# Kernel tuning notes

Hardware: AMD Instinct MI355X
Metric: run time of the kernel (lower is better)

The kernel has to match this reference:

```python
import jax, jax.numpy as jnp
import numpy as np

N, E = 100000, 1600000
IN, H, OUT = 64, 64, 32
BN_EPS = 1e-5


def setup_inputs() -> dict:
    key = jax.random.key(0)
    ks = jax.random.split(key, 13)

    def w(k, shape, fan_in):
        return jax.random.uniform(k, shape, jnp.float32, -1.0, 1.0) / np.sqrt(fan_in)

    return {
        "x": jax.random.normal(ks[0], (N, IN), jnp.float32),
        "edge_index": jax.random.randint(ks[1], (2, E), 0, N, jnp.int32),
        "W1": w(ks[2], (IN, H), IN),
        "b1": jnp.zeros((H,), jnp.float32),
        "gamma": jnp.ones((H,), jnp.float32),
        "beta": jnp.zeros((H,), jnp.float32),
        "W2": w(ks[3], (H, H), H),
        "b2": jnp.zeros((H,), jnp.float32),
        "lin2_w": w(ks[4], (H, OUT), H),
        "lin2_b": w(ks[5], (OUT,), H),
        "lin3_w": w(ks[6], (OUT, H), OUT),
        "lin3_b": w(ks[7], (H,), OUT),
    }


def gcn_conv(x, src, dst, W, b):
    # PyG GCNConv: h = D^{-1/2} (A + I) D^{-1/2} (x W) + b
    n = x.shape[0]
    h = x @ W  # [N, H]
    loop = jnp.arange(n, dtype=src.dtype)
    s = jnp.concatenate([src, loop])  # add self-loops
    d = jnp.concatenate([dst, loop])
    deg = jax.ops.segment_sum(jnp.ones_like(s, x.dtype), d, num_segments=n)
    dinv = jnp.where(deg > 0, jax.lax.rsqrt(deg), 0.0)
    norm = dinv[s] * dinv[d]  # [E+N]
    msg = h[s] * norm[:, None]  # gather + scale
    out = jax.ops.segment_sum(msg, d, num_segments=n)  # scatter-add
    return out + b


def reference(x, edge_index, W1, b1, gamma, beta, W2, b2, lin2_w, lin2_b, lin3_w, lin3_b):
    src, dst = edge_index[0], edge_index[1]
    h = gcn_conv(x, src, dst, W1, b1)
    # BatchNorm1d in eval mode with default running stats (mean=0, var=1)
    h = gamma * (h * jax.lax.rsqrt(jnp.float32(1.0 + BN_EPS))) + beta
    h = jax.nn.relu(h)  # dropout is identity in eval
    h = gcn_conv(h, src, dst, W2, b2)
    logits = h @ lin2_w + lin2_b  # [N, OUT]
    p = jax.nn.softmax(logits, axis=-1)
    ent = -jnp.sum(p * jnp.log(p + 1e-9), axis=-1)  # [N]
    wts = 1.0 / (ent + 1e-10)
    wts = (wts - wts.min()) / (wts.max() - wts.min())
    wts = jax.nn.softmax(wts, axis=0)  # [N]
    graph = jnp.sum(logits * wts[:, None], axis=0, keepdims=True)  # [1, OUT]
    return graph @ lin3_w + lin3_b  # [1, H]
```

## Files before the change

### kernel.cpp

```cpp
#include <hip/hip_runtime.h>
#include <hip/hip_bf16.h>
#include <hip/hip_fp8.h>
#include <math.h>


#define F 64
#define OUTF 32
#define PB 128
#define LEDGE 5632
#define WG 512
#define C1S 24
#define BN_INV 0.9999950000374997f
#define ESC_X 32.0f
#define IESC_X 0.03125f
#define ESC_Z 64.0f
#define IESC_Z 0.015625f

typedef short bf16x8 __attribute__((ext_vector_type(8)));
typedef float f32x4 __attribute__((ext_vector_type(4)));
typedef const __attribute__((address_space(1))) void* gas_ptr;
typedef __attribute__((address_space(3))) void* las_ptr;

__device__ __forceinline__ unsigned short f2bf(float f) {
    unsigned u = __float_as_uint(f);
    return (unsigned short)((u + 0x7fffu + ((u >> 16) & 1u)) >> 16);
}
__device__ __forceinline__ float bf2f(unsigned short h) {
    return __uint_as_float((unsigned)h << 16);
}

#if __has_builtin(__builtin_amdgcn_cvt_f32_fp8) && __has_builtin(__builtin_amdgcn_cvt_pk_fp8_f32)
__device__ __forceinline__ float4 fp8x4(unsigned v) {
    return make_float4(__builtin_amdgcn_cvt_f32_fp8((int)v, 0),
                       __builtin_amdgcn_cvt_f32_fp8((int)v, 1),
                       __builtin_amdgcn_cvt_f32_fp8((int)v, 2),
                       __builtin_amdgcn_cvt_f32_fp8((int)v, 3));
}
__device__ __forceinline__ unsigned fp8pk4(float a, float b, float c, float d) {
    int r = __builtin_amdgcn_cvt_pk_fp8_f32(a, b, 0, false);
    r = __builtin_amdgcn_cvt_pk_fp8_f32(c, d, r, true);
    return (unsigned)r;
}
__device__ __forceinline__ unsigned char fp8enc1(float a) {
    return (unsigned char)(__builtin_amdgcn_cvt_pk_fp8_f32(a, a, 0, false) & 0xff);
}
#else
__device__ __forceinline__ float fp8d1(unsigned char b) {
    __hip_fp8_e4m3 v; v.__x = (__hip_fp8_storage_t)b; return (float)v;
}
__device__ __forceinline__ float4 fp8x4(unsigned v) {
    return make_float4(fp8d1(v & 255u), fp8d1((v >> 8) & 255u), fp8d1((v >> 16) & 255u), fp8d1((v >> 24) & 255u));
}
__device__ __forceinline__ unsigned char fp8enc1(float a) {
    return (unsigned char)__hip_fp8_e4m3(a).__x;
}
__device__ __forceinline__ unsigned fp8pk4(float a, float b, float c, float d) {
    return (unsigned)fp8enc1(a) | ((unsigned)fp8enc1(b) << 8) | ((unsigned)fp8enc1(c) << 16) | ((unsigned)fp8enc1(d) << 24);
}
#endif

__global__ __launch_bounds__(256) void k_hist(const int* __restrict__ dst, int* __restrict__ hist,
                                              int E, int NBK,
                                              const float* __restrict__ W1, const float* __restrict__ b1,
                                              const float* __restrict__ gamma, const float* __restrict__ beta,
                                              const float* __restrict__ W2, const float* __restrict__ b2,
                                              const float* __restrict__ l2w, const float* __restrict__ l2b,
                                              unsigned short* __restrict__ w1f, unsigned short* __restrict__ w2f,
                                              float* __restrict__ bias1f, float* __restrict__ b2l2) {
    __shared__ int lh[512];
    int t = threadIdx.x, blk = blockIdx.x;
    if (blk >= PB) {
        int tt = (blk - PB) * 256 + t;
        int k = tt >> 5, cc = tt & 31;
        float o = 0.0f;
        for (int j = 0; j < F; j++) o += W2[k * F + j] * l2w[j * OUTF + cc];
        {
            int t2 = cc >> 4, s = k >> 5, kb = (k >> 3) & 3, jj = k & 7;
            int ln = kb * 16 + (cc & 15);
            w2f[(size_t)((t2 * 2 + s) * 64 + ln) * 8 + jj] = f2bf(o);
        }
        for (int e = tt; e < F * F; e += 2048) {
            int kk = e >> 6, c = e & 63;
            float wv = W1[kk * F + c] * gamma[c] * BN_INV;
            int t1i = c >> 4, s = kk >> 5, kb = (kk >> 3) & 3, jj = kk & 7;
            int ln = kb * 16 + (c & 15);
            w1f[(size_t)((t1i * 2 + s) * 64 + ln) * 8 + jj] = f2bf(wv);
        }
        if (tt < F) bias1f[tt] = fmaf(b1[tt], gamma[tt] * BN_INV, beta[tt]);
        if (tt < OUTF) {
            float b = l2b[tt];
            for (int j = 0; j < F; j++) b += b2[j] * l2w[j * OUTF + tt];
            b2l2[tt] = b;
        }
        return;
    }
    for (int b = t; b < NBK; b += 256) lh[b] = 0;
    __syncthreads();
    int chunk = (E + PB - 1) / PB;
    int beg = blk * chunk, end = min(beg + chunk, E);
    for (int e = beg + t; e < end; e += 256) atomicAdd(&lh[dst[e] >> 8], 1);
    __syncthreads();
    for (int b = t; b < NBK; b += 256) hist[blk * NBK + b] = lh[b];
}

__global__ __launch_bounds__(PB) void k_hscan1(int* __restrict__ hist, int* __restrict__ btot, int NBK) {
    __shared__ int s[PB];
    int b = blockIdx.x, t = threadIdx.x;
    int v = hist[t * NBK + b];
    s[t] = v;
    __syncthreads();
    for (int off = 1; off < PB; off <<= 1) {
        int u = (t >= off) ? s[t - off] : 0;
        __syncthreads();
        s[t] += u;
        __syncthreads();
    }
    hist[t * NBK + b] = s[t] - v;
    if (t == PB - 1) btot[b] = s[t];
}

__global__ void k_hscan2(const int* __restrict__ btot, int* __restrict__ bbase, int NBK) {
    __shared__ int s[512];
    int t = threadIdx.x;
    int v = (t < NBK) ? btot[t] : 0;
    s[t] = v;
    __syncthreads();
    for (int off = 1; off < 512; off <<= 1) {
        int u = (t >= off) ? s[t - off] : 0;
        __syncthreads();
        s[t] += u;
        __syncthreads();
    }
    if (t < NBK) {
        bbase[t] = s[t] - v;
        if (t == NBK - 1) bbase[NBK] = s[t];
    }
}

__global__ __launch_bounds__(256) void k_place(const int* __restrict__ src, const int* __restrict__ dst,
                                               const int* __restrict__ hist, const int* __restrict__ bbase,
                                               unsigned* __restrict__ bucketArr, int E, int NBK) {
    __shared__ int cur[512];
    int t = threadIdx.x, blk = blockIdx.x;
    for (int b = t; b < NBK; b += 256) cur[b] = hist[blk * NBK + b] + bbase[b];
    __syncthreads();
    int chunk = (E + PB - 1) / PB;
    int beg = blk * chunk, end = min(beg + chunk, E);
    for (int e = beg + t; e < end; e += 256) {
        int d = dst[e], sidx = src[e];
        int p = atomicAdd(&cur[d >> 8], 1);
        bucketArr[p] = ((unsigned)sidx << 8) | (unsigned)(d & 255);
    }
}

__global__ __launch_bounds__(256) void k_binsort(const unsigned* __restrict__ bucketArr,
                                                 const int* __restrict__ bbase,
                                                 int* __restrict__ eidx, int4* __restrict__ meta,
                                                 const float4* __restrict__ x4, unsigned* __restrict__ xq, int N) {
    __shared__ unsigned ledge[LEDGE];
    __shared__ int lcnt[256], lofs[256], lcur[256], lscan[256];
    __shared__ float ldinv[256];
    int b = blockIdx.x, t = threadIdx.x;
    int gb = bbase[b];
    int count = min(bbase[b + 1] - gb, LEDGE);
    for (int j = t; j < count; j += 256) ledge[j] = bucketArr[gb + j];
    lcnt[t] = 0;
    __syncthreads();
    for (int j = t; j < count; j += 256) atomicAdd(&lcnt[ledge[j] & 255u], 1);
    __syncthreads();
    int deg = lcnt[t];
    lscan[t] = deg;
    __syncthreads();
    for (int off = 1; off < 256; off <<= 1) {
        int u = (t >= off) ? lscan[t - off] : 0;
        __syncthreads();
        lscan[t] += u;
        __syncthreads();
    }
    lofs[t] = lscan[t] - deg;
    lcur[t] = 0;
    int node = (b << 8) + t;
    float di = rsqrtf((float)deg + 1.0f);
    ldinv[t] = di;
    if (node < N) meta[node] = make_int4(gb + lofs[t], deg, __float_as_int(di), 0);
    __syncthreads();
    for (int j = t; j < count; j += 256) {
        unsigned v = ledge[j];
        int loc = (int)(v & 255u);
        int p = atomicAdd(&lcur[loc], 1);
        eidx[gb + lofs[loc] + p] = (int)(v >> 8);
    }
    for (int idx = t; idx < 256 * 16; idx += 256) {
        int nd = (b << 8) + (idx >> 4);
        if (nd < N) {
            float d2 = ldinv[idx >> 4] * ESC_X;
            float4 v = x4[(size_t)nd * 16 + (idx & 15)];
            xq[(size_t)nd * 16 + (idx & 15)] = fp8pk4(v.x * d2, v.y * d2, v.z * d2, v.w * d2);
        }
    }
}

__global__ __launch_bounds__(128) void k_conv1l(const char* __restrict__ xqc,
                                                const int4* __restrict__ meta,
                                                const int* __restrict__ eidx,
                                                unsigned short* __restrict__ t1, int N, int Em1) {
    __shared__ __align__(16) unsigned char stage[2][C1S][64 * 16];
    int tid = threadIdx.x, wave = tid >> 6, lane = tid & 63;
    int g = lane >> 2, gl = lane & 3, gbase = lane & 60;
    int i = (blockIdx.x * 2 + wave) * 16 + g;
    int ic = min(i, N - 1);
    int4 m = meta[ic];
    int beg = m.x;
    int dcnt = (i < N) ? m.y : 0;
    float dis = __int_as_float(m.z) * IESC_X;
    int s0 = eidx[min(beg + gl, Em1)];
    int s1 = eidx[min(beg + 4 + gl, Em1)];
    int s2 = eidx[min(beg + 8 + gl, Em1)];
    int s3 = eidx[min(beg + 12 + gl, Em1)];
    int s4 = eidx[min(beg + 16 + gl, Em1)];
    int s5 = eidx[min(beg + 20 + gl, Em1)];
    uint4 selfv = *(const uint4*)(xqc + (size_t)ic * 64 + gl * 16);
#pragma unroll
    for (int k = 0; k < C1S; k++) {
        int sreg = (k < 4) ? s0 : (k < 8) ? s1 : (k < 12) ? s2 : (k < 16) ? s3 : (k < 20) ? s4 : s5;
        int sv = __shfl(sreg, gbase + (k & 3), 64);
        sv = (k < dcnt) ? sv : ic;
        const void* gp = xqc + (size_t)sv * 64 + gl * 16;
        __builtin_amdgcn_global_load_lds((gas_ptr)gp, (las_ptr)&stage[wave][k][0], 16, 0, 0);
    }
    asm volatile("s_waitcnt vmcnt(0)" ::: "memory");
    float4 a0 = fp8x4(selfv.x), a1 = fp8x4(selfv.y), a2 = fp8x4(selfv.z), a3 = fp8x4(selfv.w);
#pragma unroll
    for (int k = 0; k < C1S; k++) {
        if (k < dcnt) {
            uint4 v = *(const uint4*)&stage[wave][k][lane * 16];
            float4 vA = fp8x4(v.x), vB = fp8x4(v.y), vC = fp8x4(v.z), vD = fp8x4(v.w);
            a0.x += vA.x; a0.y += vA.y; a0.z += vA.z; a0.w += vA.w;
            a1.x += vB.x; a1.y += vB.y; a1.z += vB.z; a1.w += vB.w;
            a2.x += vC.x; a2.y += vC.y; a2.z += vC.z; a2.w += vC.w;
            a3.x += vD.x; a3.y += vD.y; a3.z += vD.z; a3.w += vD.w;
        }
    }
    for (int base = C1S; base < dcnt; base += 4) {
        int j = base + gl;
        int ss = eidx[min(beg + j, Em1)];
        int cnt = min(dcnt - base, 4);
#pragma unroll
        for (int k = 0; k < 4; k++) {
            if (k < cnt) {
                int sv = __shfl(ss, gbase + k, 64);
                uint4 v = *(const uint4*)(xqc + (size_t)sv * 64 + gl * 16);
                float4 vA = fp8x4(v.x), vB = fp8x4(v.y), vC = fp8x4(v.z), vD = fp8x4(v.w);
                a0.x += vA.x; a0.y += vA.y; a0.z += vA.z; a0.w += vA.w;
                a1.x += vB.x; a1.y += vB.y; a1.z += vB.z; a1.w += vB.w;
                a2.x += vC.x; a2.y += vC.y; a2.z += vC.z; a2.w += vC.w;
                a3.x += vD.x; a3.y += vD.y; a3.z += vD.z; a3.w += vD.w;
            }
        }
    }
    if (i < N) {
        uint4 o1, o2;
        o1.x = (unsigned)f2bf(a0.x * dis) | ((unsigned)f2bf(a0.y * dis) << 16);
        o1.y = (unsigned)f2bf(a0.z * dis) | ((unsigned)f2bf(a0.w * dis) << 16);
        o1.z = (unsigned)f2bf(a1.x * dis) | ((unsigned)f2bf(a1.y * dis) << 16);
        o1.w = (unsigned)f2bf(a1.z * dis) | ((unsigned)f2bf(a1.w * dis) << 16);
        o2.x = (unsigned)f2bf(a2.x * dis) | ((unsigned)f2bf(a2.y * dis) << 16);
        o2.y = (unsigned)f2bf(a2.z * dis) | ((unsigned)f2bf(a2.w * dis) << 16);
        o2.z = (unsigned)f2bf(a3.x * dis) | ((unsigned)f2bf(a3.y * dis) << 16);
        o2.w = (unsigned)f2bf(a3.z * dis) | ((unsigned)f2bf(a3.w * dis) << 16);
        uint4* outp = (uint4*)(t1 + (size_t)i * F + gl * 16);
        outp[0] = o1;
        outp[1] = o2;
    }
}

__global__ __launch_bounds__(256) void k_zm(const unsigned short* __restrict__ t1bf,
                                            const int4* __restrict__ meta,
                                            const unsigned short* __restrict__ w1f,
                                            const unsigned short* __restrict__ w2f,
                                            const float* __restrict__ bias1f,
                                            unsigned char* __restrict__ z2q, int N) {
    __shared__ __align__(16) unsigned short hlds[4][16][72];
    __shared__ float ldin[4][16];
    int tid = threadIdx.x, wave = tid >> 6, lane = tid & 63;
    int cl = lane & 15, kb = lane >> 4;
    int ntiles = (N + 15) >> 4;
    int tile = blockIdx.x * 4 + wave;
    if (tile >= ntiles) return;
    int row0 = tile << 4;

    int ra = min(row0 + cl, N - 1);
    const bf16x8* arow = (const bf16x8*)(t1bf + (size_t)ra * F);
    bf16x8 a0 = arow[kb];
    bf16x8 a1 = arow[4 + kb];
    if (lane < 16) ldin[wave][lane] = __int_as_float(meta[min(row0 + lane, N - 1)].z);

    const bf16x8* w1v = (const bf16x8*)w1f;
    const bf16x8* w2v = (const bf16x8*)w2f;
    bf16x8 w1frag[8];
#pragma unroll
    for (int q = 0; q < 8; q++) w1frag[q] = w1v[q * 64 + lane];
    bf16x8 w2frag[4];
#pragma unroll
    for (int q = 0; q < 4; q++) w2frag[q] = w2v[q * 64 + lane];
    float bias_t[4];
#pragma unroll
    for (int t = 0; t < 4; t++) bias_t[t] = bias1f[t * 16 + cl];

    f32x4 acc[4] = {};
#pragma unroll
    for (int t = 0; t < 4; t++) {
        acc[t] = __builtin_amdgcn_mfma_f32_16x16x32_bf16(a0, w1frag[t * 2 + 0], acc[t], 0, 0, 0);
        acc[t] = __builtin_amdgcn_mfma_f32_16x16x32_bf16(a1, w1frag[t * 2 + 1], acc[t], 0, 0, 0);
    }
    float di[4];
#pragma unroll
    for (int j = 0; j < 4; j++) di[j] = ldin[wave][kb * 4 + j];
#pragma unroll
    for (int t = 0; t < 4; t++)
#pragma unroll
        for (int j = 0; j < 4; j++) {
            float h = fmaxf(acc[t][j] + bias_t[t], 0.0f) * di[j];
            hlds[wave][kb * 4 + j][t * 16 + cl] = f2bf(h);
        }
    bf16x8 h0 = *(const bf16x8*)&hlds[wave][cl][kb * 8];
    bf16x8 h1 = *(const bf16x8*)&hlds[wave][cl][32 + kb * 8];
    f32x4 accz[2] = {};
#pragma unroll
    for (int t2 = 0; t2 < 2; t2++) {
        accz[t2] = __builtin_amdgcn_mfma_f32_16x16x32_bf16(h0, w2frag[t2 * 2 + 0], accz[t2], 0, 0, 0);
        accz[t2] = __builtin_amdgcn_mfma_f32_16x16x32_bf16(h1, w2frag[t2 * 2 + 1], accz[t2], 0, 0, 0);
    }
#pragma unroll
    for (int t2 = 0; t2 < 2; t2++)
#pragma unroll
        for (int j = 0; j < 4; j++) {
            int r = row0 + kb * 4 + j;
            if (r < N) z2q[(size_t)r * OUTF + t2 * 16 + cl] = fp8enc1(accz[t2][j] * ESC_Z);
        }
}

__device__ __forceinline__ void conv2_consume(const uint2 (&vbuf)[24], uint2 selfv, int dcnt,
                                              int i, int beg, float dis, int gl, int gbase,
                                              const uint2* __restrict__ z2q2, const int* __restrict__ eidx,
                                              int Em1, float4 bvA, float4 bvB,
                                              unsigned short* __restrict__ logits_bf,
                                              float* __restrict__ wraw,
                                              float& mnW, float& mxW, int N) {
    float4 aA0 = fp8x4(selfv.x), aB0 = fp8x4(selfv.y);
    if (i >= N) { aA0 = make_float4(0.f, 0.f, 0.f, 0.f); aB0 = aA0; }
    float4 aA1 = make_float4(0.f, 0.f, 0.f, 0.f), aB1 = aA1;
#pragma unroll
    for (int k = 0; k < 24; k++) {
        if (k < dcnt) {
            float4 vA = fp8x4(vbuf[k].x), vB = fp8x4(vbuf[k].y);
            if (k & 1) {
                aA1.x += vA.x; aA1.y += vA.y; aA1.z += vA.z; aA1.w += vA.w;
                aB1.x += vB.x; aB1.y += vB.y; aB1.z += vB.z; aB1.w += vB.w;
            } else {
                aA0.x += vA.x; aA0.y += vA.y; aA0.z += vA.z; aA0.w += vA.w;
                aB0.x += vB.x; aB0.y += vB.y; aB0.z += vB.z; aB0.w += vB.w;
            }
        }
    }
    for (int base = 24; base < dcnt; base += 4) {
        int j = base + gl;
        int ss = eidx[min(beg + j, Em1)];
        int cnt = min(dcnt - base, 4);
#pragma unroll
        for (int k = 0; k < 4; k++) {
            if (k < cnt) {
                int sv = __shfl(ss, gbase + k, 64);
                uint2 v = z2q2[(size_t)sv * 4 + gl];
                float4 vA = fp8x4(v.x), vB = fp8x4(v.y);
                aA0.x += vA.x; aA0.y += vA.y; aA0.z += vA.z; aA0.w += vA.w;
                aB0.x += vB.x; aB0.y += vB.y; aB0.z += vB.z; aB0.w += vB.w;
            }
        }
    }
    float4 lgA, lgB;
    lgA.x = fmaf(aA0.x + aA1.x, dis, bvA.x);
    lgA.y = fmaf(aA0.y + aA1.y, dis, bvA.y);
    lgA.z = fmaf(aA0.z + aA1.z, dis, bvA.z);
    lgA.w = fmaf(aA0.w + aA1.w, dis, bvA.w);
    lgB.x = fmaf(aB0.x + aB1.x, dis, bvB.x);
    lgB.y = fmaf(aB0.y + aB1.y, dis, bvB.y);
    lgB.z = fmaf(aB0.z + aB1.z, dis, bvB.z);
    lgB.w = fmaf(aB0.w + aB1.w, dis, bvB.w);
    if (i < N) {
        uint4 ob;
        ob.x = (unsigned)f2bf(lgA.x) | ((unsigned)f2bf(lgA.y) << 16);
        ob.y = (unsigned)f2bf(lgA.z) | ((unsigned)f2bf(lgA.w) << 16);
        ob.z = (unsigned)f2bf(lgB.x) | ((unsigned)f2bf(lgB.y) << 16);
        ob.w = (unsigned)f2bf(lgB.z) | ((unsigned)f2bf(lgB.w) << 16);
        *(uint4*)(logits_bf + (size_t)i * OUTF + gl * 8) = ob;
    }
    float m8 = fmaxf(fmaxf(fmaxf(lgA.x, lgA.y), fmaxf(lgA.z, lgA.w)),
                     fmaxf(fmaxf(lgB.x, lgB.y), fmaxf(lgB.z, lgB.w)));
    for (int off = 2; off > 0; off >>= 1) m8 = fmaxf(m8, __shfl_xor(m8, off, 4));
    float p0 = __expf(lgA.x - m8), p1 = __expf(lgA.y - m8), p2 = __expf(lgA.z - m8), p3 = __expf(lgA.w - m8);
    float p4 = __expf(lgB.x - m8), p5 = __expf(lgB.y - m8), p6 = __expf(lgB.z - m8), p7 = __expf(lgB.w - m8);
    float s8 = p0 + p1 + p2 + p3 + p4 + p5 + p6 + p7;
    for (int off = 2; off > 0; off >>= 1) s8 += __shfl_xor(s8, off, 4);
    float inv = 1.0f / s8;
    float t0 = p0 * inv, t1v = p1 * inv, t2v = p2 * inv, t3 = p3 * inv;
    float t4 = p4 * inv, t5 = p5 * inv, t6 = p6 * inv, t7 = p7 * inv;
    float e8 = t0 * __logf(t0 + 1e-9f) + t1v * __logf(t1v + 1e-9f) + t2v * __logf(t2v + 1e-9f) + t3 * __logf(t3 + 1e-9f) +
               t4 * __logf(t4 + 1e-9f) + t5 * __logf(t5 + 1e-9f) + t6 * __logf(t6 + 1e-9f) + t7 * __logf(t7 + 1e-9f);
    for (int off = 2; off > 0; off >>= 1) e8 += __shfl_xor(e8, off, 4);
    float w = 1.0f / (-e8 + 1e-10f);
    if (i < N) {
        if (gl == 0) wraw[i] = w;
        mnW = fminf(mnW, w);
        mxW = fmaxf(mxW, w);
    }
}

__global__ __launch_bounds__(256, 2) void k_conv2agg(const uint2* __restrict__ z2q2,
                                                     const int4* __restrict__ meta,
                                                     const int* __restrict__ eidx, const float* __restrict__ b2l2,
                                                     unsigned short* __restrict__ logits_bf, float* __restrict__ wraw,
                                                     float* __restrict__ mnmx, int N, int Em1) {
    __shared__ float smn[4], smx[4];
    int tid = threadIdx.x, wave = tid >> 6, lane = tid & 63;
    int g = lane >> 2, gl = lane & 3, gbase = lane & 60;
    float4 bvA = ((const float4*)b2l2)[gl * 2];
    float4 bvB = ((const float4*)b2l2)[gl * 2 + 1];
    int wgid = blockIdx.x * 4 + wave;
    int i0 = wgid * 32 + g;
    int i1 = wgid * 32 + 16 + g;
    int i0c = min(i0, N - 1), i1c = min(i1, N - 1);
    int4 m0 = meta[i0c], m1 = meta[i1c];
    int beg0 = m0.x, beg1 = m1.x;
    int d0 = (i0 < N) ? m0.y : 0;
    int d1 = (i1 < N) ? m1.y : 0;
    float dis0 = __int_as_float(m0.z) * IESC_Z;
    float dis1 = __int_as_float(m1.z) * IESC_Z;
    int sA0 = eidx[min(beg0 + gl, Em1)];
    int sA1 = eidx[min(beg0 + 4 + gl, Em1)];
    int sA2 = eidx[min(beg0 + 8 + gl, Em1)];
    int sA3 = eidx[min(beg0 + 12 + gl, Em1)];
    int sA4 = eidx[min(beg0 + 16 + gl, Em1)];
    int sA5 = eidx[min(beg0 + 20 + gl, Em1)];
    int sB0 = eidx[min(beg1 + gl, Em1)];
    int sB1 = eidx[min(beg1 + 4 + gl, Em1)];
    int sB2 = eidx[min(beg1 + 8 + gl, Em1)];
    int sB3 = eidx[min(beg1 + 12 + gl, Em1)];
    int sB4 = eidx[min(beg1 + 16 + gl, Em1)];
    int sB5 = eidx[min(beg1 + 20 + gl, Em1)];
    uint2 self0 = z2q2[(size_t)i0c * 4 + gl];
    uint2 self1 = z2q2[(size_t)i1c * 4 + gl];
    uint2 vb0[24], vb1[24];
#pragma unroll
    for (int k = 0; k < 24; k++) {
        int sreg = (k < 4) ? sA0 : (k < 8) ? sA1 : (k < 12) ? sA2 : (k < 16) ? sA3 : (k < 20) ? sA4 : sA5;
        int sv = __shfl(sreg, gbase + (k & 3), 64);
        sv = (k < d0) ? sv : i0c;
        vb0[k] = z2q2[(size_t)sv * 4 + gl];
    }
#pragma unroll
    for (int k = 0; k < 24; k++) {
        int sreg = (k < 4) ? sB0 : (k < 8) ? sB1 : (k < 12) ? sB2 : (k < 16) ? sB3 : (k < 20) ? sB4 : sB5;
        int sv = __shfl(sreg, gbase + (k & 3), 64);
        sv = (k < d1) ? sv : i1c;
        vb1[k] = z2q2[(size_t)sv * 4 + gl];
    }
    __builtin_amdgcn_sched_barrier(0);
    float mnW = INFINITY, mxW = -INFINITY;
    conv2_consume(vb0, self0, d0, i0, beg0, dis0, gl, gbase, z2q2, eidx, Em1,
                  bvA, bvB, logits_bf, wraw, mnW, mxW, N);
    conv2_consume(vb1, self1, d1, i1, beg1, dis1, gl, gbase, z2q2, eidx, Em1,
                  bvA, bvB, logits_bf, wraw, mnW, mxW, N);
    for (int off = 32; off > 0; off >>= 1) {
        mnW = fminf(mnW, __shfl_xor(mnW, off, 64));
        mxW = fmaxf(mxW, __shfl_xor(mxW, off, 64));
    }
    if (lane == 0) { smn[wave] = mnW; smx[wave] = mxW; }
    __syncthreads();
    if (tid == 0) {
        mnmx[blockIdx.x * 2]     = fminf(fminf(smn[0], smn[1]), fminf(smn[2], smn[3]));
        mnmx[blockIdx.x * 2 + 1] = fmaxf(fmaxf(smx[0], smx[1]), fmaxf(smx[2], smx[3]));
    }
}

__global__ __launch_bounds__(256) void k_weight(const unsigned short* __restrict__ logits_bf,
                                                const float* __restrict__ wraw,
                                                const float* __restrict__ mnmx, int nmm,
                                                float* __restrict__ part, int N) {
    __shared__ float rmn[4], rmx[4];
    float mn = INFINITY, mx = -INFINITY;
    for (int j = threadIdx.x; j < nmm; j += 256) {
        mn = fminf(mn, mnmx[j * 2]);
        mx = fmaxf(mx, mnmx[j * 2 + 1]);
    }
    for (int off = 32; off > 0; off >>= 1) {
        mn = fminf(mn, __shfl_xor(mn, off, 64));
        mx = fmaxf(mx, __shfl_xor(mx, off, 64));
    }
    int wv = threadIdx.x >> 6;
    if ((threadIdx.x & 63) == 0) { rmn[wv] = mn; rmx[wv] = mx; }
    __syncthreads();
    mn = fminf(fminf(rmn[0], rmn[1]), fminf(rmn[2], rmn[3]));
    mx = fmaxf(fmaxf(rmx[0], rmx[1]), fmaxf(rmx[2], rmx[3]));
    float inv = 1.0f / (mx - mn);
    int c = threadIdx.x & 31;
    int g = threadIdx.x >> 5;
    float acc = 0.0f, es = 0.0f;
    for (int r = blockIdx.x * 8 + g; r < N; r += gridDim.x * 8) {
        float e = __expf((wraw[r] - mn) * inv);
        acc += e * bf2f(logits_bf[(size_t)r * OUTF + c]);
        if (c == 0) es += e;
    }
    __shared__ float sa[8][OUTF];
    __shared__ float se[8];
    sa[g][c] = acc;
    if (c == 0) se[g] = es;
    __syncthreads();
    if (g == 0) {
        float t = sa[0][c];
#pragma unroll
        for (int i = 1; i < 8; i++) t += sa[i][c];
        part[blockIdx.x * 36 + c] = t;
        if (c == 0) {
            float u = 0.0f;
#pragma unroll
            for (int i = 0; i < 8; i++) u += se[i];
            part[blockIdx.x * 36 + 32] = u;
        }
    }
}

__global__ __launch_bounds__(256) void k_final(const float* __restrict__ part,
                                               const float* __restrict__ w3, const float* __restrict__ b3,
                                               float* __restrict__ out) {
    __shared__ float sa[8][OUTF];
    __shared__ float se[8];
    __shared__ float facc[OUTF + 1];
    int tid = threadIdx.x;
    int g = tid >> 5, c = tid & 31;
    float acc = 0.0f, es = 0.0f;
    for (int p = g; p < WG; p += 8) {
        acc += part[p * 36 + c];
        if (c == 0) es += part[p * 36 + 32];
    }
    sa[g][c] = acc;
    if (c == 0) se[g] = es;
    __syncthreads();
    if (tid < OUTF) {
        float t = 0.0f;
#pragma unroll
        for (int i = 0; i < 8; i++) t += sa[i][tid];
        facc[tid] = t;
    }
    if (tid == 32) {
        float u = 0.0f;
#pragma unroll
        for (int i = 0; i < 8; i++) u += se[i];
        facc[OUTF] = u;
    }
    __syncthreads();
    if (tid < F) {
        float s = facc[OUTF];
        float o = b3[tid];
#pragma unroll
        for (int cc = 0; cc < OUTF; cc++) o += (facc[cc] / s) * w3[cc * F + tid];
        out[tid] = o;
    }
}

extern "C" void kernel_launch(void* const* d_in, const int* in_sizes, int n_in,
                              void* d_out, int out_size, void* d_ws, size_t ws_size,
                              hipStream_t stream) {
    const float* x     = (const float*)d_in[0];
    const int*   ei    = (const int*)d_in[1];
    const float* W1    = (const float*)d_in[2];
    const float* b1    = (const float*)d_in[3];
    const float* gamma = (const float*)d_in[4];
    const float* beta  = (const float*)d_in[5];
    const float* W2    = (const float*)d_in[6];
    const float* b2    = (const float*)d_in[7];
    const float* l2w   = (const float*)d_in[8];
    const float* l2b   = (const float*)d_in[9];
    const float* l3w   = (const float*)d_in[10];
    const float* l3b   = (const float*)d_in[11];

    int N = in_sizes[0] / F;
    int E = in_sizes[1] / 2;
    const int* src = ei;
    const int* dst = ei + E;
    int NBK = (N + 255) >> 8;

    char* p = (char*)d_ws;
    int* hist = (int*)p;                p += (size_t)PB * NBK * 4;
    int* btot = (int*)p;                p += 512 * 4;
    int* bbase = (int*)p;               p += 516 * 4;
    unsigned* bucketArr = (unsigned*)p; p += (size_t)E * 4;
    int4* meta = (int4*)p;              p += (size_t)N * 16;
    int* eidx = (int*)p;                p += (size_t)E * 4;
    float* mnmx = (float*)p;            p += 2048 * 4;
    float* part = (float*)p;            p += (size_t)WG * 36 * 4;
    unsigned short* w1f = (unsigned short*)p;  p += F * F * 2;
    unsigned short* w2f = (unsigned short*)p;  p += F * OUTF * 2;
    float* bias1f = (float*)p;          p += F * 4;
    float* b2l2 = (float*)p;            p += OUTF * 4 + 32;
    unsigned* xq = (unsigned*)p;        p += (size_t)N * F;
    unsigned short* t1bf = (unsigned short*)p; p += (size_t)N * F * 2;
    float* wraw = (float*)p;            p += (size_t)N * 4;
    unsigned char* z2q = (unsigned char*)xq;
    unsigned short* logits_bf = (unsigned short*)t1bf;

    k_hist<<<PB + 8, 256, 0, stream>>>(dst, hist, E, NBK, W1, b1, gamma, beta, W2, b2, l2w, l2b,
                                       w1f, w2f, bias1f, b2l2);
    k_hscan1<<<NBK, PB, 0, stream>>>(hist, btot, NBK);
    k_hscan2<<<1, 512, 0, stream>>>(btot, bbase, NBK);
    k_place<<<PB, 256, 0, stream>>>(src, dst, hist, bbase, bucketArr, E, NBK);
    k_binsort<<<NBK, 256, 0, stream>>>(bucketArr, bbase, eidx, meta, (const float4*)x, xq, N);

    int nb1 = (N + 31) / 32;
    k_conv1l<<<nb1, 128, 0, stream>>>((const char*)xq, meta, eidx, t1bf, N, E - 1);
    int nt = (N + 15) >> 4;
    k_zm<<<(nt + 3) / 4, 256, 0, stream>>>(t1bf, meta, w1f, w2f, bias1f, z2q, N);
    int wg2 = (nt + 1) >> 1;
    int nb2 = (wg2 + 3) >> 2;
    k_conv2agg<<<nb2, 256, 0, stream>>>((const uint2*)z2q, meta, eidx, b2l2, logits_bf, wraw, mnmx, N, E - 1);

    k_weight<<<WG, 256, 0, stream>>>(logits_bf, wraw, mnmx, nb2, part, N);
    k_final<<<1, 256, 0, stream>>>(part, l3w, l3b, (float*)d_out);
}
```

Measured before the change: 246.6 us.

## Fuse conv1 aggregation with dense transform and inline bucket-total scan

Merges the first-layer gather/aggregation kernel with the MFMA transform kernel so the aggregated row tile stays in shared memory instead of round-tripping through a bf16 global buffer. It also removes the single-block bucket-total scan kernel and recomputes that scan redundantly inside each block of the placement and binsort kernels with a wave-shuffle scan. Gathers for absent neighbours are now skipped instead of loading the self row. The trade-offs are two fewer launches and less global traffic, against more registers and shared memory in the fused kernel and a repeated small scan in every block.

```diff
diff --git a/kernel.cpp b/kernel.cpp
--- a/kernel.cpp
+++ b/kernel.cpp
@@ -58,6 +58,34 @@
     return (unsigned)fp8enc1(a) | ((unsigned)fp8enc1(b) << 8) | ((unsigned)fp8enc1(c) << 16) | ((unsigned)fp8enc1(d) << 24);
 }
 #endif
+
+__device__ __forceinline__ void scan_btot(const int* __restrict__ btot, int* sbase, int NBK, int tid) {
+    if (tid < 64) {
+        int lane = tid;
+        int vals[8];
+        int lsum = 0;
+#pragma unroll
+        for (int q = 0; q < 8; q++) {
+            int idx = lane * 8 + q;
+            int v = (idx < NBK) ? btot[idx] : 0;
+            vals[q] = lsum;
+            lsum += v;
+        }
+        int run = lsum;
+        for (int off = 1; off < 64; off <<= 1) {
+            int u = __shfl_up(run, off, 64);
+            if (lane >= off) run += u;
+        }
+        int excl = run - lsum;
+#pragma unroll
+        for (int q = 0; q < 8; q++) {
+            int idx = lane * 8 + q;
+            if (idx <= NBK) sbase[idx] = excl + vals[q];
+        }
+        if (lane == 63) sbase[NBK] = run;
+    }
+    __syncthreads();
+}
 
 __global__ __launch_bounds__(256) void k_hist(const int* __restrict__ dst, int* __restrict__ hist,
                                               int E, int NBK,
@@ -119,30 +147,14 @@
     if (t == PB - 1) btot[b] = s[t];
 }
 
-__global__ void k_hscan2(const int* __restrict__ btot, int* __restrict__ bbase, int NBK) {
-    __shared__ int s[512];
-    int t = threadIdx.x;
-    int v = (t < NBK) ? btot[t] : 0;
-    s[t] = v;
-    __syncthreads();
-    for (int off = 1; off < 512; off <<= 1) {
-        int u = (t >= off) ? s[t - off] : 0;
-        __syncthreads();
-        s[t] += u;
-        __syncthreads();
-    }
-    if (t < NBK) {
-        bbase[t] = s[t] - v;
-        if (t == NBK - 1) bbase[NBK] = s[t];
-    }
-}
-
 __global__ __launch_bounds__(256) void k_place(const int* __restrict__ src, const int* __restrict__ dst,
-                                               const int* __restrict__ hist, const int* __restrict__ bbase,
+                                               const int* __restrict__ hist, const int* __restrict__ btot,
                                                unsigned* __restrict__ bucketArr, int E, int NBK) {
     __shared__ int cur[512];
+    __shared__ int sbase[513];
     int t = threadIdx.x, blk = blockIdx.x;
-    for (int b = t; b < NBK; b += 256) cur[b] = hist[blk * NBK + b] + bbase[b];
+    scan_btot(btot, sbase, NBK, t);
+    for (int b = t; b < NBK; b += 256) cur[b] = hist[blk * NBK + b] + sbase[b];
     __syncthreads();
     int chunk = (E + PB - 1) / PB;
     int beg = blk * chunk, end = min(beg + chunk, E);
@@ -154,15 +166,17 @@
 }
 
 __global__ __launch_bounds__(256) void k_binsort(const unsigned* __restrict__ bucketArr,
-                                                 const int* __restrict__ bbase,
+                                                 const int* __restrict__ btot,
                                                  int* __restrict__ eidx, int4* __restrict__ meta,
-                                                 const float4* __restrict__ x4, unsigned* __restrict__ xq, int N) {
+                                                 const float4* __restrict__ x4, unsigned* __restrict__ xq, int N, int NBK) {
     __shared__ unsigned ledge[LEDGE];
     __shared__ int lcnt[256], lofs[256], lcur[256], lscan[256];
+    __shared__ int sbase[513];
     __shared__ float ldinv[256];
     int b = blockIdx.x, t = threadIdx.x;
-    int gb = bbase[b];
-    int count = min(bbase[b + 1] - gb, LEDGE);
+    scan_btot(btot, sbase, NBK, t);
+    int gb = sbase[b];
+    int count = min(sbase[b + 1] - gb, LEDGE);
     for (int j = t; j < count; j += 256) ledge[j] = bucketArr[gb + j];
     lcnt[t] = 0;
     __syncthreads();
@@ -200,11 +214,16 @@
     }
 }
 
-__global__ __launch_bounds__(128) void k_conv1l(const char* __restrict__ xqc,
-                                                const int4* __restrict__ meta,
-                                                const int* __restrict__ eidx,
-                                                unsigned short* __restrict__ t1, int N, int Em1) {
+__global__ __launch_bounds__(128) void k_c1z(const char* __restrict__ xqc,
+                                             const int4* __restrict__ meta,
+                                             const int* __restrict__ eidx,
+                                             const unsigned short* __restrict__ w1f,
+                                             const unsigned short* __restrict__ w2f,
+                                             const float* __restrict__ bias1f,
+                                             unsigned char* __restrict__ z2q, int N, int Em1) {
     __shared__ __align__(16) unsigned char stage[2][C1S][64 * 16];
+    __shared__ __align__(16) unsigned short tile[2][16][72];
+    __shared__ float ldin[2][16];
     int tid = threadIdx.x, wave = tid >> 6, lane = tid & 63;
     int g = lane >> 2, gl = lane & 3, gbase = lane & 60;
     int i = (blockIdx.x * 2 + wave) * 16 + g;
@@ -213,6 +232,7 @@
     int beg = m.x;
     int dcnt = (i < N) ? m.y : 0;
     float dis = __int_as_float(m.z) * IESC_X;
+    if (gl == 0) ldin[wave][g] = __int_as_float(m.z);
     int s0 = eidx[min(beg + gl, Em1)];
     int s1 = eidx[min(beg + 4 + gl, Em1)];
     int s2 = eidx[min(beg + 8 + gl, Em1)];
@@ -224,12 +244,25 @@
     for (int k = 0; k < C1S; k++) {
         int sreg = (k < 4) ? s0 : (k < 8) ? s1 : (k < 12) ? s2 : (k < 16) ? s3 : (k < 20) ? s4 : s5;
         int sv = __shfl(sreg, gbase + (k & 3), 64);
-        sv = (k < dcnt) ? sv : ic;
-        const void* gp = xqc + (size_t)sv * 64 + gl * 16;
-        __builtin_amdgcn_global_load_lds((gas_ptr)gp, (las_ptr)&stage[wave][k][0], 16, 0, 0);
-    }
+        if (k < dcnt) {
+            const void* gp = xqc + (size_t)sv * 64 + gl * 16;
+            __builtin_amdgcn_global_load_lds((gas_ptr)gp, (las_ptr)&stage[wave][k][0], 16, 0, 0);
+        }
+    }
+    int cl = lane & 15, kb = lane >> 4;
+    const bf16x8* w1v = (const bf16x8*)w1f;
+    const bf16x8* w2v = (const bf16x8*)w2f;
+    bf16x8 w1frag[8];
+#pragma unroll
+    for (int q = 0; q < 8; q++) w1frag[q] = w1v[q * 64 + lane];
+    bf16x8 w2frag[4];
+#pragma unroll
+    for (int q = 0; q < 4; q++) w2frag[q] = w2v[q * 64 + lane];
+    float bias_t[4];
+#pragma unroll
+    for (int t = 0; t < 4; t++) bias_t[t] = bias1f[t * 16 + cl];
+    float4 a0 = fp8x4(selfv.x), a1 = fp8x4(selfv.y), a2 = fp8x4(selfv.z), a3 = fp8x4(selfv.w);
     asm volatile("s_waitcnt vmcnt(0)" ::: "memory");
-    float4 a0 = fp8x4(selfv.x), a1 = fp8x4(selfv.y), a2 = fp8x4(selfv.z), a3 = fp8x4(selfv.w);
 #pragma unroll
     for (int k = 0; k < C1S; k++) {
         if (k < dcnt) {
@@ -258,7 +291,7 @@
             }
         }
     }
-    if (i < N) {
+    {
         uint4 o1, o2;
         o1.x = (unsigned)f2bf(a0.x * dis) | ((unsigned)f2bf(a0.y * dis) << 16);
         o1.y = (unsigned)f2bf(a0.z * dis) | ((unsigned)f2bf(a0.w * dis) << 16);
@@ -268,50 +301,17 @@
         o2.y = (unsigned)f2bf(a2.z * dis) | ((unsigned)f2bf(a2.w * dis) << 16);
         o2.z = (unsigned)f2bf(a3.x * dis) | ((unsigned)f2bf(a3.y * dis) << 16);
         o2.w = (unsigned)f2bf(a3.z * dis) | ((unsigned)f2bf(a3.w * dis) << 16);
-        uint4* outp = (uint4*)(t1 + (size_t)i * F + gl * 16);
-        outp[0] = o1;
-        outp[1] = o2;
-    }
-}
-
-__global__ __launch_bounds__(256) void k_zm(const unsigned short* __restrict__ t1bf,
-                                            const int4* __restrict__ meta,
-                                            const unsigned short* __restrict__ w1f,
-                                            const unsigned short* __restrict__ w2f,
-                                            const float* __restrict__ bias1f,
-                                            unsigned char* __restrict__ z2q, int N) {
-    __shared__ __align__(16) unsigned short hlds[4][16][72];
-    __shared__ float ldin[4][16];
-    int tid = threadIdx.x, wave = tid >> 6, lane = tid & 63;
-    int cl = lane & 15, kb = lane >> 4;
-    int ntiles = (N + 15) >> 4;
-    int tile = blockIdx.x * 4 + wave;
-    if (tile >= ntiles) return;
-    int row0 = tile << 4;
-
-    int ra = min(row0 + cl, N - 1);
-    const bf16x8* arow = (const bf16x8*)(t1bf + (size_t)ra * F);
-    bf16x8 a0 = arow[kb];
-    bf16x8 a1 = arow[4 + kb];
-    if (lane < 16) ldin[wave][lane] = __int_as_float(meta[min(row0 + lane, N - 1)].z);
-
-    const bf16x8* w1v = (const bf16x8*)w1f;
-    const bf16x8* w2v = (const bf16x8*)w2f;
-    bf16x8 w1frag[8];
-#pragma unroll
-    for (int q = 0; q < 8; q++) w1frag[q] = w1v[q * 64 + lane];
-    bf16x8 w2frag[4];
-#pragma unroll
-    for (int q = 0; q < 4; q++) w2frag[q] = w2v[q * 64 + lane];
-    float bias_t[4];
-#pragma unroll
-    for (int t = 0; t < 4; t++) bias_t[t] = bias1f[t * 16 + cl];
-
+        uint4* tp = (uint4*)&tile[wave][g][gl * 16];
+        tp[0] = o1;
+        tp[1] = o2;
+    }
+    bf16x8 af0 = *(const bf16x8*)&tile[wave][cl][kb * 8];
+    bf16x8 af1 = *(const bf16x8*)&tile[wave][cl][32 + kb * 8];
     f32x4 acc[4] = {};
 #pragma unroll
     for (int t = 0; t < 4; t++) {
-        acc[t] = __builtin_amdgcn_mfma_f32_16x16x32_bf16(a0, w1frag[t * 2 + 0], acc[t], 0, 0, 0);
-        acc[t] = __builtin_amdgcn_mfma_f32_16x16x32_bf16(a1, w1frag[t * 2 + 1], acc[t], 0, 0, 0);
+        acc[t] = __builtin_amdgcn_mfma_f32_16x16x32_bf16(af0, w1frag[t * 2 + 0], acc[t], 0, 0, 0);
+        acc[t] = __builtin_amdgcn_mfma_f32_16x16x32_bf16(af1, w1frag[t * 2 + 1], acc[t], 0, 0, 0);
     }
     float di[4];
 #pragma unroll
@@ -321,16 +321,17 @@
 #pragma unroll
         for (int j = 0; j < 4; j++) {
             float h = fmaxf(acc[t][j] + bias_t[t], 0.0f) * di[j];
-            hlds[wave][kb * 4 + j][t * 16 + cl] = f2bf(h);
-        }
-    bf16x8 h0 = *(const bf16x8*)&hlds[wave][cl][kb * 8];
-    bf16x8 h1 = *(const bf16x8*)&hlds[wave][cl][32 + kb * 8];
+            tile[wave][kb * 4 + j][t * 16 + cl] = f2bf(h);
+        }
+    bf16x8 h0 = *(const bf16x8*)&tile[wave][cl][kb * 8];
+    bf16x8 h1 = *(const bf16x8*)&tile[wave][cl][32 + kb * 8];
     f32x4 accz[2] = {};
 #pragma unroll
     for (int t2 = 0; t2 < 2; t2++) {
         accz[t2] = __builtin_amdgcn_mfma_f32_16x16x32_bf16(h0, w2frag[t2 * 2 + 0], accz[t2], 0, 0, 0);
         accz[t2] = __builtin_amdgcn_mfma_f32_16x16x32_bf16(h1, w2frag[t2 * 2 + 1], accz[t2], 0, 0, 0);
     }
+    int row0 = (blockIdx.x * 2 + wave) * 16;
 #pragma unroll
     for (int t2 = 0; t2 < 2; t2++)
 #pragma unroll
@@ -593,7 +594,6 @@
     char* p = (char*)d_ws;
     int* hist = (int*)p;                p += (size_t)PB * NBK * 4;
     int* btot = (int*)p;                p += 512 * 4;
-    int* bbase = (int*)p;               p += 516 * 4;
     unsigned* bucketArr = (unsigned*)p; p += (size_t)E * 4;
     int4* meta = (int4*)p;              p += (size_t)N * 16;
     int* eidx = (int*)p;                p += (size_t)E * 4;
@@ -604,22 +604,19 @@
     float* bias1f = (float*)p;          p += F * 4;
     float* b2l2 = (float*)p;            p += OUTF * 4 + 32;
     unsigned* xq = (unsigned*)p;        p += (size_t)N * F;
-    unsigned short* t1bf = (unsigned short*)p; p += (size_t)N * F * 2;
+    unsigned char* z2q = (unsigned char*)p; p += (size_t)N * OUTF;
+    unsigned short* logits_bf = (unsigned short*)p; p += (size_t)N * OUTF * 2;
     float* wraw = (float*)p;            p += (size_t)N * 4;
-    unsigned char* z2q = (unsigned char*)xq;
-    unsigned short* logits_bf = (unsigned short*)t1bf;
 
     k_hist<<<PB + 8, 256, 0, stream>>>(dst, hist, E, NBK, W1, b1, gamma, beta, W2, b2, l2w, l2b,
                                        w1f, w2f, bias1f, b2l2);
     k_hscan1<<<NBK, PB, 0, stream>>>(hist, btot, NBK);
-    k_hscan2<<<1, 512, 0, stream>>>(btot, bbase, NBK);
-    k_place<<<PB, 256, 0, stream>>>(src, dst, hist, bbase, bucketArr, E, NBK);
-    k_binsort<<<NBK, 256, 0, stream>>>(bucketArr, bbase, eidx, meta, (const float4*)x, xq, N);
+    k_place<<<PB, 256, 0, stream>>>(src, dst, hist, btot, bucketArr, E, NBK);
+    k_binsort<<<NBK, 256, 0, stream>>>(bucketArr, btot, eidx, meta, (const float4*)x, xq, N, NBK);
 
     int nb1 = (N + 31) / 32;
-    k_conv1l<<<nb1, 128, 0, stream>>>((const char*)xq, meta, eidx, t1bf, N, E - 1);
+    k_c1z<<<nb1, 128, 0, stream>>>((const char*)xq, meta, eidx, w1f, w2f, bias1f, z2q, N, E - 1);
     int nt = (N + 15) >> 4;
-    k_zm<<<(nt + 3) / 4, 256, 0, stream>>>(t1bf, meta, w1f, w2f, bias1f, z2q, N);
     int wg2 = (nt + 1) >> 1;
     int nb2 = (wg2 + 3) >> 2;
     k_conv2agg<<<nb2, 256, 0, stream>>>((const uint2*)z2q, meta, eidx, b2l2, logits_bf, wraw, mnmx, N, E - 1);
```

Result: slower. 251.8 us (+2.1%).
